# Performance work log

Measured on AMD Instinct MI355X. Metric: run time of the kernel, lower is better.

## Reference

```python
import jax, jax.numpy as jnp
import numpy as np

L_MAX = 6
R = 1
IN_IRREPS  = [(256,0),(128,1),(128,2),(64,3),(64,4),(64,5),(64,6)]
HID_IRREPS = [(64,0),(64,1),(64,2),(32,3),(32,4),(32,5),(32,6)]
N_SCALARS = 64
N_GATES = sum(m for m, l in HID_IRREPS if l > 0)  # 256
PRE_IRREPS = [(N_SCALARS,0),(N_GATES,0)] + [(m,l) for m,l in HID_IRREPS if l > 0]
OUT_IRREPS = [(R,l) for l in range(L_MAX+1)]

def _dim(irr):
    return sum(m*(2*l+1) for m, l in irr)

def _wsize(in_irr, out_irr):
    mul_in = {l: m for m, l in in_irr}
    return sum(mul_in[l]*mo for mo, l in out_irr)

def e3linear(x, wflat, in_irr, out_irr):
    # block-diagonal per-irrep linear with e3nn 1/sqrt(fan_in) normalization
    B = x.shape[0]
    blocks = {}
    off = 0
    for mul, l in in_irr:
        d = mul*(2*l+1)
        blocks[l] = (x[:, off:off+d].reshape(B, mul, 2*l+1), mul)
        off += d
    outs = []
    woff = 0
    for mul_out, l in out_irr:
        xb, mul_in = blocks[l]
        w = wflat[woff:woff+mul_in*mul_out].reshape(mul_in, mul_out)
        woff += mul_in*mul_out
        y = jnp.einsum('bim,io->bom', xb, w) * (1.0/np.sqrt(mul_in))
        outs.append(y.reshape(B, mul_out*(2*l+1)))
    return jnp.concatenate(outs, axis=1)

def gate(z):
    # z = [scalars 64x0e | gates 256x0e | gated l>0 irreps]
    s = jax.nn.silu(z[:, :N_SCALARS])
    g = jax.nn.sigmoid(z[:, N_SCALARS:N_SCALARS+N_GATES])
    x = z[:, N_SCALARS+N_GATES:]
    outs = [s]
    goff = 0
    xoff = 0
    for mul, l in HID_IRREPS:
        if l == 0:
            continue
        m = 2*l+1
        xb = x[:, xoff:xoff+mul*m].reshape(-1, mul, m)
        outs.append((xb * g[:, goff:goff+mul, None]).reshape(-1, mul*m))
        goff += mul
        xoff += mul*m
    return jnp.concatenate(outs, axis=1)

def _forward(v_raw, w1, w2, w3, w4):
    x = gate(e3linear(v_raw, w1, IN_IRREPS, PRE_IRREPS))
    x = gate(e3linear(x, w2, HID_IRREPS, PRE_IRREPS))
    x = gate(e3linear(x, w3, HID_IRREPS, PRE_IRREPS))
    c = e3linear(x, w4, HID_IRREPS, OUT_IRREPS)  # [B, 49]
    B = c.shape[0]
    segs = []
    off = 0
    for l in range(L_MAX+1):
        m = 2*l+1
        seg = c[:, off:off+R*m].reshape(B, R, m).transpose(0, 2, 1)  # (B, m, R)
        segs.append(seg)
        off += R*m
    return jnp.concatenate(segs, axis=1)  # (B, 49, R)

def setup_inputs():
    key = jax.random.key(0)
    ks = jax.random.split(key, 5)
    B = 16384
    return {
        "v_raw": jax.random.normal(ks[0], (B, _dim(IN_IRREPS)), jnp.float32),
        "w1": jax.random.normal(ks[1], (_wsize(IN_IRREPS, PRE_IRREPS),), jnp.float32),
        "w2": jax.random.normal(ks[2], (_wsize(HID_IRREPS, PRE_IRREPS),), jnp.float32),
        "w3": jax.random.normal(ks[3], (_wsize(HID_IRREPS, PRE_IRREPS),), jnp.float32),
        "w4": jax.random.normal(ks[4], (_wsize(HID_IRREPS, OUT_IRREPS),), jnp.float32),
    }

def reference(v_raw, w1, w2, w3, w4):
    return _forward(v_raw, w1, w2, w3, w4)
```

## Files before the change

kernel.cpp:

```cpp
#include <hip/hip_runtime.h>
#include <cstddef>


typedef _Float16 half8 __attribute__((ext_vector_type(8)));
typedef _Float16 half4 __attribute__((ext_vector_type(4)));
typedef float    f32x4 __attribute__((ext_vector_type(4)));
typedef float    fvec4 __attribute__((ext_vector_type(4)));

#define B_ROWS   8
#define IN_DIM   3840
#define OUT_COLS 49

#define OFF_STG  0
#define OFF_HA   8064
#define OFF_HB   12544
#define OFF_HSA  17024
#define OFF_HSB  18176
#define OFF_G1   19328
#define OFF_G2   21440
#define OFF_G3   23552
#define SMEM_ELTS 25664

#define P2BASE 106496
#define P3BASE 139264

__global__ __launch_bounds__(256) void prep_weights(
    const float* __restrict__ w1, const float* __restrict__ w2,
    const float* __restrict__ w3, _Float16* __restrict__ packed)
{
  static const int K_[24]    = {256,256,128,128,64,64,64,64,  64,64,64,64,32,32,32,32,
                                64,64,64,64,32,32,32,32};
  static const int N_[24]    = {64,256,64,64,32,32,32,32,  64,256,64,64,32,32,32,32,
                                64,256,64,64,32,32,32,32};
  static const int woff_[24] = {0,16384,81920,90112,98304,100352,102400,104448,
                                0,4096,20480,24576,28672,29696,30720,31744,
                                0,4096,20480,24576,28672,29696,30720,31744};
  static const int poff_[24] = {0,16384,81920,90112,98304,100352,102400,104448,
                                106496,110592,126976,131072,135168,136192,137216,138240,
                                139264,143360,159744,163840,167936,168960,169984,171008};
  const int g = blockIdx.x * 256 + threadIdx.x;
  int bi = 0;
#pragma unroll
  for (int i = 1; i < 24; ++i) if (g * 8 >= poff_[i]) bi = i;
  const float* w = (bi < 8) ? w1 : ((bi < 16) ? w2 : w3);
  const int rel8 = g - poff_[bi] / 8;
  const int lane = rel8 & 63;
  const int fi   = rel8 >> 6;
  const int K = K_[bi], N = N_[bi];
  const int KF = K >> 5;
  const int kf = fi % KF;
  const int mt = fi / KF;
  const int k0 = kf * 32 + (lane >> 4) * 8;
  const int o  = mt * 16 + (lane & 15);
  const float scale = 1.0f / sqrtf((float)K);
  half8 vv;
#pragma unroll
  for (int j = 0; j < 8; ++j)
    vv[j] = (_Float16)(w[woff_[bi] + (size_t)(k0 + j) * N + o] * scale);
  *(half8*)(packed + (size_t)g * 8) = vv;
}

template<int TWOL1, int MUL>
__device__ __forceinline__ void issue_loads(const float* __restrict__ vraw,
                                            int b0, int inoff, fvec4 (&regs)[7])
{
  constexpr int D  = MUL * TWOL1;
  constexpr int D4 = D / 4;
  constexpr int V4 = D4 * B_ROWS;
  constexpr int NV = (V4 + 255) / 256;
  const int t = threadIdx.x;
#pragma unroll
  for (int v = 0; v < NV; ++v) {
    const int gv = v * 256 + t;
    if ((V4 & 255) == 0 || gv < V4) {
      const int b  = gv / D4;
      const int dd = (gv - b * D4) * 4;
      regs[v] = *(const fvec4*)(vraw + (size_t)(b0 + b) * IN_DIM + inoff + dd);
    }
  }
}

template<int TWOL1, int MUL>
__device__ __forceinline__ void write_stage(const fvec4 (&regs)[7], _Float16* stg)
{
  constexpr int D  = MUL * TWOL1;
  constexpr int D4 = D / 4;
  constexpr int V4 = D4 * B_ROWS;
  constexpr int NV = (V4 + 255) / 256;
  constexpr int KP = MUL + 8;
  const int t = threadIdx.x;
#pragma unroll
  for (int v = 0; v < NV; ++v) {
    const int gv = v * 256 + t;
    if ((V4 & 255) == 0 || gv < V4) {
      const int b  = gv / D4;
      const int dd = (gv - b * D4) * 4;
      const fvec4 x = regs[v];
#pragma unroll
      for (int j = 0; j < 4; ++j) {
        const int d = dd + j;
        const int i = d / TWOL1;
        const int m = d - i * TWOL1;
        stg[(b * TWOL1 + m) * KP + i] = (_Float16)x[j];
      }
    }
  }
}

__device__ __forceinline__ void ws_l0(const fvec4 (&regs)[7], _Float16* stg)
{
  const int t = threadIdx.x;
#pragma unroll
  for (int v = 0; v < 2; ++v) {
    const int gv = v * 256 + t;
    const int b  = gv >> 6;
    const int i0 = (gv & 63) * 4;
    const fvec4 x = regs[v];
    half4 h;
#pragma unroll
    for (int j = 0; j < 4; ++j) h[j] = (_Float16)x[j];
    *(half4*)(stg + b * 264 + i0) = h;
  }
}

template<int TWOL1, int K, int N>
__device__ __forceinline__ void gemm_sw(
    const _Float16* __restrict__ Bact, const _Float16* __restrict__ Ap,
    _Float16* __restrict__ H, const _Float16* __restrict__ G, int goff)
{
  constexpr int R  = 8 * TWOL1;
  constexpr int NT = (R + 15) / 16;
  constexpr int MT = N / 16;
  constexpr int KF = K / 32;
  constexpr int AP = K + 8;
  constexpr int HP = N + 8;
  const int lane = threadIdx.x & 63;
  const int wave = threadIdx.x >> 6;
  const int col  = lane & 15;
  const int quad = lane >> 4;
  for (int t = wave; t < MT * NT; t += 4) {
    const int mt = t % MT;
    const int nt = t / MT;
    f32x4 acc = {0.f, 0.f, 0.f, 0.f};
    const _Float16* bp = Bact + (nt * 16 + col) * AP + quad * 8;
    const _Float16* ap = Ap + ((size_t)(mt * KF * 64 + lane)) * 8;
#pragma unroll
    for (int kf = 0; kf < KF; ++kf) {
      const half8 av = *(const half8*)(ap + kf * 512);
      const half8 bv = *(const half8*)(bp + kf * 32);
      acc = __builtin_amdgcn_mfma_f32_16x16x32_f16(av, bv, acc, 0, 0, 0);
    }
    const int c = nt * 16 + col;
    if (c < R) {
      const int b  = c / TWOL1;
      const int o0 = mt * 16 + quad * 4;
      const half4 g4 = *(const half4*)(G + b * 264 + goff + o0);
      half4 hv;
#pragma unroll
      for (int r = 0; r < 4; ++r) hv[r] = (_Float16)(acc[r] * (float)g4[r]);
      *(half4*)(H + c * HP + o0) = hv;
    }
  }
}

template<int K>
__device__ __forceinline__ void scal_sw(
    const _Float16* __restrict__ Bact, const _Float16* __restrict__ ApS,
    const _Float16* __restrict__ ApG, _Float16* __restrict__ HsOut,
    _Float16* __restrict__ Gout)
{
  constexpr int KF = K / 32;
  constexpr int AP = K + 8;
  const int lane = threadIdx.x & 63;
  const int wave = threadIdx.x >> 6;
  const int col  = lane & 15;
  const int quad = lane >> 4;
  const _Float16* bp = Bact + col * AP + quad * 8;
  {
    const int mt = wave;
    f32x4 acc = {0.f, 0.f, 0.f, 0.f};
    const _Float16* ap = ApS + ((size_t)(mt * KF * 64 + lane)) * 8;
#pragma unroll
    for (int kf = 0; kf < KF; ++kf)
      acc = __builtin_amdgcn_mfma_f32_16x16x32_f16(
          *(const half8*)(ap + kf * 512), *(const half8*)(bp + kf * 32), acc, 0, 0, 0);
    if (col < B_ROWS) {
      const int o0 = mt * 16 + quad * 4;
      half4 hv;
#pragma unroll
      for (int r = 0; r < 4; ++r) {
        const float z = acc[r];
        hv[r] = (_Float16)(z * __builtin_amdgcn_rcpf(1.f + __expf(-z)));
      }
      *(half4*)(HsOut + col * 72 + o0) = hv;
    }
  }
  for (int mt = wave; mt < 16; mt += 4) {
    f32x4 acc = {0.f, 0.f, 0.f, 0.f};
    const _Float16* ap = ApG + ((size_t)(mt * KF * 64 + lane)) * 8;
#pragma unroll
    for (int kf = 0; kf < KF; ++kf)
      acc = __builtin_amdgcn_mfma_f32_16x16x32_f16(
          *(const half8*)(ap + kf * 512), *(const half8*)(bp + kf * 32), acc, 0, 0, 0);
    if (col < B_ROWS) {
      const int o0 = mt * 16 + quad * 4;
      half4 gv;
#pragma unroll
      for (int r = 0; r < 4; ++r)
        gv[r] = (_Float16)__builtin_amdgcn_rcpf(1.f + __expf(-acc[r]));
      *(half4*)(Gout + col * 264 + o0) = gv;
    }
  }
}

template<int TWOL1, int K>
__device__ __forceinline__ void layer4_sw(
    const _Float16* __restrict__ H, const float* __restrict__ w4, int w4off,
    float* __restrict__ out, int b0, int lsq)
{
  constexpr int R  = 8 * TWOL1;
  constexpr int HP = K + 8;
  const int r = threadIdx.x;
  if (r < R) {
    float s = 0.f;
#pragma unroll
    for (int i8 = 0; i8 < K / 8; ++i8) {
      const half8 hv = *(const half8*)(H + r * HP + i8 * 8);
#pragma unroll
      for (int j = 0; j < 8; ++j) s += (float)hv[j] * w4[w4off + i8 * 8 + j];
    }
    constexpr float scale = (K == 64) ? 0.125f : 0.17677669529663687f;
    out[(size_t)(b0 + r / TWOL1) * OUT_COLS + lsq + (r % TWOL1)] = s * scale;
  }
}

__global__ __launch_bounds__(256, 3) void fused_decoder(
    const float* __restrict__ vraw, const float* __restrict__ w4,
    const _Float16* __restrict__ packed, float* __restrict__ out)
{
  __shared__ __align__(16) _Float16 smem[SMEM_ELTS];
  _Float16* STG = smem + OFF_STG;
  _Float16* HA  = smem + OFF_HA;
  _Float16* HB  = smem + OFF_HB;
  _Float16* HsA = smem + OFF_HSA;
  _Float16* HsB = smem + OFF_HSB;
  _Float16* G1  = smem + OFF_G1;
  _Float16* G2  = smem + OFF_G2;
  _Float16* G3  = smem + OFF_G3;
  const int b0 = blockIdx.x * B_ROWS;
  const _Float16* pk = packed;
  fvec4 rA[7], rB[7];

  issue_loads<1, 256>(vraw, b0, 0, rA);
  issue_loads<3, 128>(vraw, b0, 256, rB);
  ws_l0(rA, STG);
  __syncthreads();
  scal_sw<256>(STG, pk + 0, pk + 16384, HsA, G1);
  __syncthreads();
  write_stage<3, 128>(rB, STG);
  issue_loads<5, 128>(vraw, b0, 640, rA);
  scal_sw<64>(HsA, pk + P2BASE, pk + P2BASE + 4096, HsB, G2);
  __syncthreads();
  scal_sw<64>(HsB, pk + P3BASE, pk + P3BASE + 4096, HsA, G3);
  __syncthreads();
  layer4_sw<1, 64>(HsA, w4, 0, out, b0, 0);
  gemm_sw<3, 128, 64>(STG, pk + 81920, HA, G1, 0);
  __syncthreads();
  write_stage<5, 128>(rA, STG);
  issue_loads<7, 64>(vraw, b0, 1280, rB);
  gemm_sw<3, 64, 64>(HA, pk + P2BASE + 20480, HB, G2, 0);
  __syncthreads();
  gemm_sw<3, 64, 64>(HB, pk + P3BASE + 20480, HA, G3, 0);
  __syncthreads();
  layer4_sw<3, 64>(HA, w4, 64, out, b0, 1);
  gemm_sw<5, 128, 64>(STG, pk + 90112, HB, G1, 64);
  __syncthreads();
  write_stage<7, 64>(rB, STG);
  issue_loads<9, 64>(vraw, b0, 1728, rA);
  gemm_sw<5, 64, 64>(HB, pk + P2BASE + 24576, HA, G2, 64);
  __syncthreads();
  gemm_sw<5, 64, 64>(HA, pk + P3BASE + 24576, HB, G3, 64);
  __syncthreads();
  layer4_sw<5, 64>(HB, w4, 128, out, b0, 4);
  gemm_sw<7, 64, 32>(STG, pk + 98304, HA, G1, 128);
  __syncthreads();
  write_stage<9, 64>(rA, STG);
  issue_loads<11, 64>(vraw, b0, 2304, rB);
  gemm_sw<7, 32, 32>(HA, pk + P2BASE + 28672, HB, G2, 128);
  __syncthreads();
  gemm_sw<7, 32, 32>(HB, pk + P3BASE + 28672, HA, G3, 128);
  __syncthreads();
  layer4_sw<7, 32>(HA, w4, 192, out, b0, 9);
  gemm_sw<9, 64, 32>(STG, pk + 100352, HB, G1, 160);
  __syncthreads();
  write_stage<11, 64>(rB, STG);
  issue_loads<13, 64>(vraw, b0, 3008, rA);
  gemm_sw<9, 32, 32>(HB, pk + P2BASE + 29696, HA, G2, 160);
  __syncthreads();
  gemm_sw<9, 32, 32>(HA, pk + P3BASE + 29696, HB, G3, 160);
  __syncthreads();
  layer4_sw<9, 32>(HB, w4, 224, out, b0, 16);
  gemm_sw<11, 64, 32>(STG, pk + 102400, HA, G1, 192);
  __syncthreads();
  write_stage<13, 64>(rA, STG);
  gemm_sw<11, 32, 32>(HA, pk + P2BASE + 30720, HB, G2, 192);
  __syncthreads();
  gemm_sw<11, 32, 32>(HB, pk + P3BASE + 30720, HA, G3, 192);
  __syncthreads();
  layer4_sw<11, 32>(HA, w4, 256, out, b0, 25);
  gemm_sw<13, 64, 32>(STG, pk + 104448, HB, G1, 224);
  __syncthreads();
  gemm_sw<13, 32, 32>(HB, pk + P2BASE + 31744, HA, G2, 224);
  __syncthreads();
  gemm_sw<13, 32, 32>(HA, pk + P3BASE + 31744, HB, G3, 224);
  __syncthreads();
  layer4_sw<13, 32>(HB, w4, 288, out, b0, 36);
}

extern "C" void kernel_launch(void* const* d_in, const int* in_sizes, int n_in,
                              void* d_out, int out_size, void* d_ws, size_t ws_size,
                              hipStream_t stream)
{
  (void)in_sizes; (void)n_in; (void)out_size; (void)ws_size;
  const float* vraw = (const float*)d_in[0];
  const float* w1   = (const float*)d_in[1];
  const float* w2   = (const float*)d_in[2];
  const float* w3   = (const float*)d_in[3];
  const float* w4   = (const float*)d_in[4];
  float* out = (float*)d_out;
  _Float16* packed = (_Float16*)d_ws;

  prep_weights<<<84, 256, 0, stream>>>(w1, w2, w3, packed);
  fused_decoder<<<16384 / B_ROWS, 256, 0, stream>>>(vraw, w4, packed, out);
}
```

Measured before the change: 391.1 us.

## Split l>0 irrep work into per-wave independent units without block barriers

Replaces the block-wide sequence of per-irrep GEMMs, each separated by __syncthreads, with per-wave work units of 16 columns. Each unit runs all three gated layers plus the final dot product inside one wave, using wave-private LDS scratch and only an lgkmcnt wait between steps. The next unit's input is loaded straight from global memory into registers while the current unit computes. Units are hand-balanced across the four waves. Without barriers, waves can progress independently, but the split may leave waves with unequal work, the input loads are strided and uncoalesced, and register pressure rises (32 floats per thread). It also swaps rcp for true division in the activations.

```diff
diff --git a/kernel.cpp b/kernel.cpp
--- a/kernel.cpp
+++ b/kernel.cpp
@@ -11,18 +11,22 @@
 #define IN_DIM   3840
 #define OUT_COLS 49
 
-#define OFF_STG  0
-#define OFF_HA   8064
-#define OFF_HB   12544
-#define OFF_HSA  17024
-#define OFF_HSB  18176
-#define OFF_G1   19328
-#define OFF_G2   21440
-#define OFF_G3   23552
-#define SMEM_ELTS 25664
+#define OFF_STG0 0
+#define OFF_HSA  4224
+#define OFF_HSB  5376
+#define OFF_G1   6528
+#define OFF_G2   8640
+#define OFF_G3   10752
+#define OFF_SW   12864
+#define OFF_H1   21568
+#define SMEM_ELTS 26176
 
 #define P2BASE 106496
 #define P3BASE 139264
+
+__device__ __forceinline__ void wave_fence() {
+  asm volatile("s_waitcnt lgkmcnt(0)" ::: "memory");
+}
 
 __global__ __launch_bounds__(256) void prep_weights(
     const float* __restrict__ w1, const float* __restrict__ w2,
@@ -60,54 +64,157 @@
   *(half8*)(packed + (size_t)g * 8) = vv;
 }
 
-template<int TWOL1, int MUL>
-__device__ __forceinline__ void issue_loads(const float* __restrict__ vraw,
-                                            int b0, int inoff, fvec4 (&regs)[7])
-{
-  constexpr int D  = MUL * TWOL1;
-  constexpr int D4 = D / 4;
-  constexpr int V4 = D4 * B_ROWS;
-  constexpr int NV = (V4 + 255) / 256;
-  const int t = threadIdx.x;
-#pragma unroll
-  for (int v = 0; v < NV; ++v) {
-    const int gv = v * 256 + t;
-    if ((V4 & 255) == 0 || gv < V4) {
-      const int b  = gv / D4;
-      const int dd = (gv - b * D4) * 4;
-      regs[v] = *(const fvec4*)(vraw + (size_t)(b0 + b) * IN_DIM + inoff + dd);
-    }
-  }
-}
-
-template<int TWOL1, int MUL>
-__device__ __forceinline__ void write_stage(const fvec4 (&regs)[7], _Float16* stg)
-{
-  constexpr int D  = MUL * TWOL1;
-  constexpr int D4 = D / 4;
-  constexpr int V4 = D4 * B_ROWS;
-  constexpr int NV = (V4 + 255) / 256;
-  constexpr int KP = MUL + 8;
-  const int t = threadIdx.x;
-#pragma unroll
-  for (int v = 0; v < NV; ++v) {
-    const int gv = v * 256 + t;
-    if ((V4 & 255) == 0 || gv < V4) {
-      const int b  = gv / D4;
-      const int dd = (gv - b * D4) * 4;
-      const fvec4 x = regs[v];
-#pragma unroll
-      for (int j = 0; j < 4; ++j) {
-        const int d = dd + j;
-        const int i = d / TWOL1;
-        const int m = d - i * TWOL1;
-        stg[(b * TWOL1 + m) * KP + i] = (_Float16)x[j];
-      }
-    }
-  }
-}
-
-__device__ __forceinline__ void ws_l0(const fvec4 (&regs)[7], _Float16* stg)
+template<int L> struct CP {
+  static constexpr int TWOL1 = 2 * L + 1;
+  static constexpr int MUL   = (L <= 2) ? 128 : 64;
+  static constexpr int N1    = (L <= 2) ? 64  : 32;
+  static constexpr int KF1   = MUL / 32;
+  static constexpr int KF2   = N1 / 32;
+  static constexpr int MT    = N1 / 16;
+  static constexpr int AP    = MUL + 8;
+  static constexpr int HP    = N1 + 8;
+  static constexpr int R     = 8 * TWOL1;
+  static constexpr int NQ    = (16 * (MUL / 4)) / 64;
+  static constexpr int INOFF = (L==1)?256:(L==2)?640:(L==3)?1280:(L==4)?1728:(L==5)?2304:3008;
+  static constexpr int P1    = (L==1)?81920:(L==2)?90112:(L==3)?98304:(L==4)?100352:(L==5)?102400:104448;
+  static constexpr int P2R   = (L==1)?20480:(L==2)?24576:(L==3)?28672:(L==4)?29696:(L==5)?30720:31744;
+  static constexpr int GO    = (L==1)?0:(L==2)?64:(L==3)?128:(L==4)?160:(L==5)?192:224;
+  static constexpr int W4O   = (L==1)?64:(L==2)?128:(L==3)?192:(L==4)?224:(L==5)?256:288;
+};
+
+template<int L, int CT>
+__device__ __forceinline__ void unit_load(const float* __restrict__ vraw,
+                                          int b0, float (&rg)[32])
+{
+  using P = CP<L>;
+  const int lane = threadIdx.x & 63;
+#pragma unroll
+  for (int v = 0; v < P::NQ; ++v) {
+    const int flat = v * 64 + lane;
+    const int cc = flat & 15;
+    const int iq = flat >> 4;
+    const int c  = CT * 16 + cc;
+    if (c < P::R) {
+      const int b = c / P::TWOL1;
+      const int m = c - b * P::TWOL1;
+      const float* base = vraw + (size_t)(b0 + b) * IN_DIM + P::INOFF + m
+                        + (size_t)(iq * 4) * P::TWOL1;
+#pragma unroll
+      for (int jj = 0; jj < 4; ++jj) rg[v * 4 + jj] = base[(size_t)jj * P::TWOL1];
+    }
+  }
+}
+
+template<int L, int CT>
+__device__ __forceinline__ void unit_stage(const float (&rg)[32], _Float16* SW)
+{
+  using P = CP<L>;
+  const int lane = threadIdx.x & 63;
+#pragma unroll
+  for (int v = 0; v < P::NQ; ++v) {
+    const int flat = v * 64 + lane;
+    const int cc = flat & 15;
+    const int iq = flat >> 4;
+    if (CT * 16 + cc < P::R) {
+      half4 h;
+#pragma unroll
+      for (int jj = 0; jj < 4; ++jj) h[jj] = (_Float16)rg[v * 4 + jj];
+      *(half4*)(SW + cc * P::AP + iq * 4) = h;
+    }
+  }
+}
+
+template<int L, int CT>
+__device__ __forceinline__ void unit_compute(
+    _Float16* SW, _Float16* H1, const _Float16* __restrict__ pk,
+    const _Float16* G1, const _Float16* G2, const _Float16* G3,
+    const float* __restrict__ w4, float* __restrict__ out, int b0)
+{
+  using P = CP<L>;
+  const int lane = threadIdx.x & 63;
+  const int col  = lane & 15;
+  const int quad = lane >> 4;
+  const int c    = CT * 16 + col;
+  const bool vc  = c < P::R;
+  const int b    = c / P::TWOL1;
+  const int m    = c - b * P::TWOL1;
+#pragma unroll
+  for (int mt = 0; mt < P::MT; ++mt) {
+    f32x4 acc = {0.f, 0.f, 0.f, 0.f};
+#pragma unroll
+    for (int kf = 0; kf < P::KF1; ++kf) {
+      const half8 av = *(const half8*)(pk + P::P1 + (size_t)((mt * P::KF1 + kf) * 64 + lane) * 8);
+      const half8 bv = *(const half8*)(SW + col * P::AP + kf * 32 + quad * 8);
+      acc = __builtin_amdgcn_mfma_f32_16x16x32_f16(av, bv, acc, 0, 0, 0);
+    }
+    if (vc) {
+      const int o0 = mt * 16 + quad * 4;
+      const half4 g4 = *(const half4*)(G1 + b * 264 + P::GO + o0);
+      half4 hv;
+#pragma unroll
+      for (int r = 0; r < 4; ++r) hv[r] = (_Float16)(acc[r] * (float)g4[r]);
+      *(half4*)(H1 + col * P::HP + o0) = hv;
+    }
+  }
+  wave_fence();
+#pragma unroll
+  for (int mt = 0; mt < P::MT; ++mt) {
+    f32x4 acc = {0.f, 0.f, 0.f, 0.f};
+#pragma unroll
+    for (int kf = 0; kf < P::KF2; ++kf) {
+      const half8 av = *(const half8*)(pk + P2BASE + P::P2R + (size_t)((mt * P::KF2 + kf) * 64 + lane) * 8);
+      const half8 bv = *(const half8*)(H1 + col * P::HP + kf * 32 + quad * 8);
+      acc = __builtin_amdgcn_mfma_f32_16x16x32_f16(av, bv, acc, 0, 0, 0);
+    }
+    if (vc) {
+      const int o0 = mt * 16 + quad * 4;
+      const half4 g4 = *(const half4*)(G2 + b * 264 + P::GO + o0);
+      half4 hv;
+#pragma unroll
+      for (int r = 0; r < 4; ++r) hv[r] = (_Float16)(acc[r] * (float)g4[r]);
+      *(half4*)(SW + col * P::HP + o0) = hv;
+    }
+  }
+  wave_fence();
+#pragma unroll
+  for (int mt = 0; mt < P::MT; ++mt) {
+    f32x4 acc = {0.f, 0.f, 0.f, 0.f};
+#pragma unroll
+    for (int kf = 0; kf < P::KF2; ++kf) {
+      const half8 av = *(const half8*)(pk + P3BASE + P::P2R + (size_t)((mt * P::KF2 + kf) * 64 + lane) * 8);
+      const half8 bv = *(const half8*)(SW + col * P::HP + kf * 32 + quad * 8);
+      acc = __builtin_amdgcn_mfma_f32_16x16x32_f16(av, bv, acc, 0, 0, 0);
+    }
+    if (vc) {
+      const int o0 = mt * 16 + quad * 4;
+      const half4 g4 = *(const half4*)(G3 + b * 264 + P::GO + o0);
+      half4 hv;
+#pragma unroll
+      for (int r = 0; r < 4; ++r) hv[r] = (_Float16)(acc[r] * (float)g4[r]);
+      *(half4*)(H1 + col * P::HP + o0) = hv;
+    }
+  }
+  wave_fence();
+  float s = 0.f;
+  if (vc) {
+    constexpr int SEG = P::N1 / 4;
+#pragma unroll
+    for (int h8 = 0; h8 < SEG / 8; ++h8) {
+      const half8 hv = *(const half8*)(H1 + col * P::HP + quad * SEG + h8 * 8);
+#pragma unroll
+      for (int j = 0; j < 8; ++j)
+        s += (float)hv[j] * w4[P::W4O + quad * SEG + h8 * 8 + j];
+    }
+  }
+  s += __shfl_xor(s, 16, 64);
+  s += __shfl_xor(s, 32, 64);
+  if (vc && quad == 0) {
+    constexpr float scale = (P::N1 == 64) ? 0.125f : 0.17677669529663687f;
+    out[(size_t)(b0 + b) * OUT_COLS + L * L + m] = s * scale;
+  }
+}
+
+__device__ __forceinline__ void ws_l0(const fvec4 (&regs)[2], _Float16* stg)
 {
   const int t = threadIdx.x;
 #pragma unroll
@@ -123,59 +230,18 @@
   }
 }
 
-template<int TWOL1, int K, int N>
-__device__ __forceinline__ void gemm_sw(
-    const _Float16* __restrict__ Bact, const _Float16* __restrict__ Ap,
-    _Float16* __restrict__ H, const _Float16* __restrict__ G, int goff)
-{
-  constexpr int R  = 8 * TWOL1;
-  constexpr int NT = (R + 15) / 16;
-  constexpr int MT = N / 16;
+template<int K>
+__device__ __forceinline__ void scal_sw(
+    const _Float16* __restrict__ Bact, const _Float16* __restrict__ ApS,
+    const _Float16* __restrict__ ApG, _Float16* __restrict__ HsOut,
+    _Float16* __restrict__ Gout, int AP_)
+{
   constexpr int KF = K / 32;
-  constexpr int AP = K + 8;
-  constexpr int HP = N + 8;
   const int lane = threadIdx.x & 63;
   const int wave = threadIdx.x >> 6;
   const int col  = lane & 15;
   const int quad = lane >> 4;
-  for (int t = wave; t < MT * NT; t += 4) {
-    const int mt = t % MT;
-    const int nt = t / MT;
-    f32x4 acc = {0.f, 0.f, 0.f, 0.f};
-    const _Float16* bp = Bact + (nt * 16 + col) * AP + quad * 8;
-    const _Float16* ap = Ap + ((size_t)(mt * KF * 64 + lane)) * 8;
-#pragma unroll
-    for (int kf = 0; kf < KF; ++kf) {
-      const half8 av = *(const half8*)(ap + kf * 512);
-      const half8 bv = *(const half8*)(bp + kf * 32);
-      acc = __builtin_amdgcn_mfma_f32_16x16x32_f16(av, bv, acc, 0, 0, 0);
-    }
-    const int c = nt * 16 + col;
-    if (c < R) {
-      const int b  = c / TWOL1;
-      const int o0 = mt * 16 + quad * 4;
-      const half4 g4 = *(const half4*)(G + b * 264 + goff + o0);
-      half4 hv;
-#pragma unroll
-      for (int r = 0; r < 4; ++r) hv[r] = (_Float16)(acc[r] * (float)g4[r]);
-      *(half4*)(H + c * HP + o0) = hv;
-    }
-  }
-}
-
-template<int K>
-__device__ __forceinline__ void scal_sw(
-    const _Float16* __restrict__ Bact, const _Float16* __restrict__ ApS,
-    const _Float16* __restrict__ ApG, _Float16* __restrict__ HsOut,
-    _Float16* __restrict__ Gout)
-{
-  constexpr int KF = K / 32;
-  constexpr int AP = K + 8;
-  const int lane = threadIdx.x & 63;
-  const int wave = threadIdx.x >> 6;
-  const int col  = lane & 15;
-  const int quad = lane >> 4;
-  const _Float16* bp = Bact + col * AP + quad * 8;
+  const _Float16* bp = Bact + col * AP_ + quad * 8;
   {
     const int mt = wave;
     f32x4 acc = {0.f, 0.f, 0.f, 0.f};
@@ -190,12 +256,14 @@
 #pragma unroll
       for (int r = 0; r < 4; ++r) {
         const float z = acc[r];
-        hv[r] = (_Float16)(z * __builtin_amdgcn_rcpf(1.f + __expf(-z)));
+        hv[r] = (_Float16)(z / (1.f + __expf(-z)));
       }
       *(half4*)(HsOut + col * 72 + o0) = hv;
     }
   }
-  for (int mt = wave; mt < 16; mt += 4) {
+#pragma unroll
+  for (int mt0 = 0; mt0 < 4; ++mt0) {
+    const int mt = mt0 * 4 + wave;
     f32x4 acc = {0.f, 0.f, 0.f, 0.f};
     const _Float16* ap = ApG + ((size_t)(mt * KF * 64 + lane)) * 8;
 #pragma unroll
@@ -207,114 +275,95 @@
       half4 gv;
 #pragma unroll
       for (int r = 0; r < 4; ++r)
-        gv[r] = (_Float16)__builtin_amdgcn_rcpf(1.f + __expf(-acc[r]));
+        gv[r] = (_Float16)(1.f / (1.f + __expf(-acc[r])));
       *(half4*)(Gout + col * 264 + o0) = gv;
     }
   }
 }
 
-template<int TWOL1, int K>
-__device__ __forceinline__ void layer4_sw(
-    const _Float16* __restrict__ H, const float* __restrict__ w4, int w4off,
-    float* __restrict__ out, int b0, int lsq)
-{
-  constexpr int R  = 8 * TWOL1;
-  constexpr int HP = K + 8;
+__device__ __forceinline__ void scalar_dot(const _Float16* __restrict__ Hs,
+                                           const float* __restrict__ w4,
+                                           float* __restrict__ out, int b0)
+{
   const int r = threadIdx.x;
-  if (r < R) {
+  if (r < B_ROWS) {
     float s = 0.f;
 #pragma unroll
-    for (int i8 = 0; i8 < K / 8; ++i8) {
-      const half8 hv = *(const half8*)(H + r * HP + i8 * 8);
-#pragma unroll
-      for (int j = 0; j < 8; ++j) s += (float)hv[j] * w4[w4off + i8 * 8 + j];
-    }
-    constexpr float scale = (K == 64) ? 0.125f : 0.17677669529663687f;
-    out[(size_t)(b0 + r / TWOL1) * OUT_COLS + lsq + (r % TWOL1)] = s * scale;
+    for (int i8 = 0; i8 < 8; ++i8) {
+      const half8 hv = *(const half8*)(Hs + r * 72 + i8 * 8);
+#pragma unroll
+      for (int j = 0; j < 8; ++j) s += (float)hv[j] * w4[i8 * 8 + j];
+    }
+    out[(size_t)(b0 + r) * OUT_COLS] = s * 0.125f;
   }
 }
 
 __global__ __launch_bounds__(256, 3) void fused_decoder(
     const float* __restrict__ vraw, const float* __restrict__ w4,
-    const _Float16* __restrict__ packed, float* __restrict__ out)
+    const _Float16* __restrict__ pk, float* __restrict__ out)
 {
   __shared__ __align__(16) _Float16 smem[SMEM_ELTS];
-  _Float16* STG = smem + OFF_STG;
-  _Float16* HA  = smem + OFF_HA;
-  _Float16* HB  = smem + OFF_HB;
-  _Float16* HsA = smem + OFF_HSA;
-  _Float16* HsB = smem + OFF_HSB;
-  _Float16* G1  = smem + OFF_G1;
-  _Float16* G2  = smem + OFF_G2;
-  _Float16* G3  = smem + OFF_G3;
+  _Float16* STG0 = smem + OFF_STG0;
+  _Float16* HsA  = smem + OFF_HSA;
+  _Float16* HsB  = smem + OFF_HSB;
+  _Float16* G1   = smem + OFF_G1;
+  _Float16* G2   = smem + OFF_G2;
+  _Float16* G3   = smem + OFF_G3;
+  const int wv = threadIdx.x >> 6;
+  _Float16* SW = smem + OFF_SW + wv * 2176;
+  _Float16* H1 = smem + OFF_H1 + wv * 1152;
   const int b0 = blockIdx.x * B_ROWS;
-  const _Float16* pk = packed;
-  fvec4 rA[7], rB[7];
-
-  issue_loads<1, 256>(vraw, b0, 0, rA);
-  issue_loads<3, 128>(vraw, b0, 256, rB);
-  ws_l0(rA, STG);
+
+  fvec4 rA[2];
+  {
+    const int t = threadIdx.x;
+#pragma unroll
+    for (int v = 0; v < 2; ++v) {
+      const int gv = v * 256 + t;
+      rA[v] = *(const fvec4*)(vraw + (size_t)(b0 + (gv >> 6)) * IN_DIM + (gv & 63) * 4);
+    }
+  }
+  float rg[32];
+  if      (wv == 0) unit_load<2,0>(vraw, b0, rg);
+  else if (wv == 1) unit_load<1,0>(vraw, b0, rg);
+  else if (wv == 2) unit_load<6,0>(vraw, b0, rg);
+  else              unit_load<5,0>(vraw, b0, rg);
+
+  ws_l0(rA, STG0);
   __syncthreads();
-  scal_sw<256>(STG, pk + 0, pk + 16384, HsA, G1);
+  scal_sw<256>(STG0, pk + 0, pk + 16384, HsA, G1, 264);
   __syncthreads();
-  write_stage<3, 128>(rB, STG);
-  issue_loads<5, 128>(vraw, b0, 640, rA);
-  scal_sw<64>(HsA, pk + P2BASE, pk + P2BASE + 4096, HsB, G2);
+  scal_sw<64>(HsA, pk + P2BASE, pk + P2BASE + 4096, HsB, G2, 72);
   __syncthreads();
-  scal_sw<64>(HsB, pk + P3BASE, pk + P3BASE + 4096, HsA, G3);
+  scal_sw<64>(HsB, pk + P3BASE, pk + P3BASE + 4096, HsA, G3, 72);
   __syncthreads();
-  layer4_sw<1, 64>(HsA, w4, 0, out, b0, 0);
-  gemm_sw<3, 128, 64>(STG, pk + 81920, HA, G1, 0);
-  __syncthreads();
-  write_stage<5, 128>(rA, STG);
-  issue_loads<7, 64>(vraw, b0, 1280, rB);
-  gemm_sw<3, 64, 64>(HA, pk + P2BASE + 20480, HB, G2, 0);
-  __syncthreads();
-  gemm_sw<3, 64, 64>(HB, pk + P3BASE + 20480, HA, G3, 0);
-  __syncthreads();
-  layer4_sw<3, 64>(HA, w4, 64, out, b0, 1);
-  gemm_sw<5, 128, 64>(STG, pk + 90112, HB, G1, 64);
-  __syncthreads();
-  write_stage<7, 64>(rB, STG);
-  issue_loads<9, 64>(vraw, b0, 1728, rA);
-  gemm_sw<5, 64, 64>(HB, pk + P2BASE + 24576, HA, G2, 64);
-  __syncthreads();
-  gemm_sw<5, 64, 64>(HA, pk + P3BASE + 24576, HB, G3, 64);
-  __syncthreads();
-  layer4_sw<5, 64>(HB, w4, 128, out, b0, 4);
-  gemm_sw<7, 64, 32>(STG, pk + 98304, HA, G1, 128);
-  __syncthreads();
-  write_stage<9, 64>(rA, STG);
-  issue_loads<11, 64>(vraw, b0, 2304, rB);
-  gemm_sw<7, 32, 32>(HA, pk + P2BASE + 28672, HB, G2, 128);
-  __syncthreads();
-  gemm_sw<7, 32, 32>(HB, pk + P3BASE + 28672, HA, G3, 128);
-  __syncthreads();
-  layer4_sw<7, 32>(HA, w4, 192, out, b0, 9);
-  gemm_sw<9, 64, 32>(STG, pk + 100352, HB, G1, 160);
-  __syncthreads();
-  write_stage<11, 64>(rB, STG);
-  issue_loads<13, 64>(vraw, b0, 3008, rA);
-  gemm_sw<9, 32, 32>(HB, pk + P2BASE + 29696, HA, G2, 160);
-  __syncthreads();
-  gemm_sw<9, 32, 32>(HA, pk + P3BASE + 29696, HB, G3, 160);
-  __syncthreads();
-  layer4_sw<9, 32>(HB, w4, 224, out, b0, 16);
-  gemm_sw<11, 64, 32>(STG, pk + 102400, HA, G1, 192);
-  __syncthreads();
-  write_stage<13, 64>(rA, STG);
-  gemm_sw<11, 32, 32>(HA, pk + P2BASE + 30720, HB, G2, 192);
-  __syncthreads();
-  gemm_sw<11, 32, 32>(HB, pk + P3BASE + 30720, HA, G3, 192);
-  __syncthreads();
-  layer4_sw<11, 32>(HA, w4, 256, out, b0, 25);
-  gemm_sw<13, 64, 32>(STG, pk + 104448, HB, G1, 224);
-  __syncthreads();
-  gemm_sw<13, 32, 32>(HB, pk + P2BASE + 31744, HA, G2, 224);
-  __syncthreads();
-  gemm_sw<13, 32, 32>(HA, pk + P3BASE + 31744, HB, G3, 224);
-  __syncthreads();
-  layer4_sw<13, 32>(HB, w4, 288, out, b0, 36);
+
+#define RUN_PF(Lc, CTc, Ln, CTn)                                   \
+  unit_stage<Lc, CTc>(rg, SW); wave_fence();                       \
+  unit_load<Ln, CTn>(vraw, b0, rg);                                \
+  unit_compute<Lc, CTc>(SW, H1, pk, G1, G2, G3, w4, out, b0);
+#define RUN_LAST(Lc, CTc)                                          \
+  unit_stage<Lc, CTc>(rg, SW); wave_fence();                       \
+  unit_compute<Lc, CTc>(SW, H1, pk, G1, G2, G3, w4, out, b0);
+
+  if (wv == 0) {
+    scalar_dot(HsA, w4, out, b0);
+    RUN_PF(2,0, 2,1); RUN_PF(2,1, 2,2); RUN_PF(2,2, 3,3);
+    RUN_LAST(3,3);
+  } else if (wv == 1) {
+    RUN_PF(1,0, 1,1); RUN_PF(1,1, 4,0); RUN_PF(4,0, 4,1);
+    RUN_PF(4,1, 4,2); RUN_LAST(4,2);
+  } else if (wv == 2) {
+    RUN_PF(6,0, 6,1); RUN_PF(6,1, 6,2); RUN_PF(6,2, 6,3);
+    RUN_PF(6,3, 6,4); RUN_PF(6,4, 6,5); RUN_PF(6,5, 6,6);
+    RUN_PF(6,6, 3,0); RUN_PF(3,0, 3,1); RUN_LAST(3,1);
+  } else {
+    RUN_PF(5,0, 5,1); RUN_PF(5,1, 5,2); RUN_PF(5,2, 5,3);
+    RUN_PF(5,3, 5,4); RUN_PF(5,4, 5,5); RUN_PF(5,5, 4,3);
+    RUN_PF(4,3, 4,4); RUN_PF(4,4, 3,2); RUN_LAST(3,2);
+  }
+#undef RUN_PF
+#undef RUN_LAST
 }
 
 extern "C" void kernel_launch(void* const* d_in, const int* in_sizes, int n_in,
```

Result: slower. 431.5 us (+10.3%).
